# Optimization experiments

Measured on AMD Instinct MI355X. Metric: run time of the kernel, lower is better.

Reference implementation:

```python
import jax, jax.numpy as jnp
import numpy as np

EPS = 1e-6
NUM_HEADS = 16

def layernorm(x, alpha, bias):
    # Faithful to the torch module: torch.std uses ddof=1, and eps is added to std.
    mean = jnp.mean(x, axis=-1, keepdims=True)
    std = jnp.std(x, axis=-1, keepdims=True, ddof=1)
    return alpha * (x - mean) / (std + EPS) + bias

def setup_inputs() -> dict:
    key = jax.random.key(0)
    B, S, D, F = 4, 2048, 1024, 4096
    ks = jax.random.split(key, 8)
    s = 1.0 / np.sqrt(D)
    inp = {
        'x': jax.random.normal(ks[0], (B, S, D), jnp.float32),
        'src_mask': jnp.ones((B, 1, 1, S), jnp.int32),
        'wq': jax.random.normal(ks[1], (D, D), jnp.float32) * s,
        'bq': jnp.zeros((D,), jnp.float32),
        'wk': jax.random.normal(ks[2], (D, D), jnp.float32) * s,
        'bk': jnp.zeros((D,), jnp.float32),
        'wv': jax.random.normal(ks[3], (D, D), jnp.float32) * s,
        'bv': jnp.zeros((D,), jnp.float32),
        'wo': jax.random.normal(ks[4], (D, D), jnp.float32) * s,
        'bo': jnp.zeros((D,), jnp.float32),
        'w1': jax.random.normal(ks[5], (D, F), jnp.float32) * s,
        'b1': jnp.zeros((F,), jnp.float32),
        'w2': jax.random.normal(ks[6], (F, D), jnp.float32) * (1.0 / np.sqrt(F)),
        'b2': jnp.zeros((D,), jnp.float32),
        'ln1_a': jnp.ones((D,), jnp.float32),
        'ln1_b': jnp.zeros((D,), jnp.float32),
        'ln2_a': jnp.ones((D,), jnp.float32),
        'ln2_b': jnp.zeros((D,), jnp.float32),
    }
    return inp

def mha(x, src_mask, wq, bq, wk, bk, wv, bv, wo, bo):
    B, S, D = x.shape
    H = NUM_HEADS
    dk = D // H
    q = (x @ wq + bq).reshape(B, S, H, dk).transpose(0, 2, 1, 3)  # [B,H,S,dk]
    k = (x @ wk + bk).reshape(B, S, H, dk).transpose(0, 2, 1, 3)
    v = (x @ wv + bv).reshape(B, S, H, dk).transpose(0, 2, 1, 3)
    scores = jnp.einsum('bhqd,bhkd->bhqk', q, k) / np.sqrt(dk)  # [B,H,S,S]
    scores = jnp.where(src_mask == 0, -1e9, scores)
    p = jax.nn.softmax(scores, axis=-1)
    ctx = jnp.einsum('bhqk,bhkd->bhqd', p, v)  # [B,H,S,dk]
    ctx = ctx.transpose(0, 2, 1, 3).reshape(B, S, D)
    return ctx @ wo + bo

def reference(x, src_mask, wq, bq, wk, bk, wv, bv, wo, bo,
              w1, b1, w2, b2, ln1_a, ln1_b, ln2_a, ln2_b):
    # residual 1: pre-norm self-attention (dropout is identity in eval)
    h = x + mha(layernorm(x, ln1_a, ln1_b), src_mask, wq, bq, wk, bk, wv, bv, wo, bo)
    # residual 2: pre-norm FFN
    hn = layernorm(h, ln2_a, ln2_b)
    ffn = jax.nn.relu(hn @ w1 + b1) @ w2 + b2
    return h + ffn
```

## Files before the change

kernel.cpp:

```cpp
#include <hip/hip_runtime.h>
#include <hip/hip_bf16.h>

typedef __attribute__((ext_vector_type(8))) short bf16x8;
typedef __attribute__((ext_vector_type(4))) short bf16x4;
typedef __attribute__((ext_vector_type(4))) float f32x4;
typedef __hip_bfloat16 bf16;
typedef unsigned short u16;

#define B_ 4
#define S_ 2048
#define D_ 1024
#define F_ 4096
#define H_ 16
#define MROWS 8192

__device__ __forceinline__ u16 f2bf_bits(float f){
  union{bf16 h; u16 u;} x; x.h = __float2bfloat16(f); return x.u;
}
__device__ __forceinline__ unsigned packbf(float a, float b){
  return (unsigned)f2bf_bits(a) | ((unsigned)f2bf_bits(b)<<16);
}
__device__ __forceinline__ void gll16(const bf16* gp, u16* lp){
  __builtin_amdgcn_global_load_lds(
      (const __attribute__((address_space(1))) void*)gp,
      (__attribute__((address_space(3))) void*)lp, 16, 0, 0);
}

struct Ptr4 { const float* p[4]; };
__global__ __launch_bounds__(256) void transpose4_to_bf16(
    Ptr4 ws_, bf16* __restrict__ WT)
{
  __shared__ float t[32][33];
  const float* W = ws_.p[blockIdx.z];
  bf16* dst = WT + (size_t)blockIdx.z*1024*1024;
  int n0 = blockIdx.x*32, k0 = blockIdx.y*32;
  int x = threadIdx.x, y = threadIdx.y;
  #pragma unroll
  for (int i=0;i<32;i+=8)
    t[y+i][x] = W[(size_t)(k0+y+i)*1024 + n0+x];
  __syncthreads();
  #pragma unroll
  for (int i=0;i<32;i+=8)
    dst[(size_t)(n0+y+i)*1024 + k0+x] = __float2bfloat16(t[x][y+i]);
}

__global__ __launch_bounds__(256) void transpose_to_bf16(
    const float* __restrict__ W, bf16* __restrict__ WT, int K, int N)
{
  __shared__ float t[32][33];
  int n0 = blockIdx.x*32, k0 = blockIdx.y*32;
  int x = threadIdx.x, y = threadIdx.y;
  #pragma unroll
  for (int i=0;i<32;i+=8)
    t[y+i][x] = W[(size_t)(k0+y+i)*N + n0+x];
  __syncthreads();
  #pragma unroll
  for (int i=0;i<32;i+=8)
    WT[(size_t)(n0+y+i)*K + k0+x] = __float2bfloat16(t[x][y+i]);
}

__global__ __launch_bounds__(256) void concat_bias(
    const float* __restrict__ bq, const float* __restrict__ bk,
    const float* __restrict__ bv, float* __restrict__ out)
{
  int i = blockIdx.x*256 + threadIdx.x;
  float v = (i < 1024) ? bq[i] : (i < 2048) ? bk[i-1024] : bv[i-2048];
  out[i] = v;
}

__global__ __launch_bounds__(256) void v_transpose(
    const bf16* __restrict__ qkv, bf16* __restrict__ vT)
{
  __shared__ u16 tile[64*65];
  const int bh = blockIdx.y, b = bh>>4, h = bh&15;
  const int s0 = blockIdx.x*64;
  const int tid = threadIdx.x;
  const bf16* src = qkv + (size_t)(b*S_ + s0)*3072 + 2048 + h*64;
  #pragma unroll
  for (int i=0;i<2;i++){
    int idx = i*256 + tid;
    int r = idx>>3, sg = idx&7;
    uint4 v = *reinterpret_cast<const uint4*>(src + (size_t)r*3072 + sg*8);
    const u16* e = (const u16*)&v;
    #pragma unroll
    for (int j=0;j<8;j++) tile[r*65 + sg*8 + j] = e[j];
  }
  __syncthreads();
  bf16* dst = vT + (size_t)bh*64*S_ + s0;
  #pragma unroll
  for (int i=0;i<2;i++){
    int idx = i*256 + tid;
    int d = idx>>3, sg = idx&7;
    u16 tmp[8];
    #pragma unroll
    for (int j=0;j<8;j++) tmp[j] = tile[(sg*8+j)*65 + d];
    *reinterpret_cast<uint4*>(dst + (size_t)d*S_ + sg*8) = *reinterpret_cast<uint4*>(tmp);
  }
}

__device__ __forceinline__ float block_reduce_256(float v, float* sbuf){
  #pragma unroll
  for (int o=32;o>0;o>>=1) v += __shfl_down(v, o);
  int wave = threadIdx.x>>6;
  if ((threadIdx.x&63)==0) sbuf[wave] = v;
  __syncthreads();
  float r = sbuf[0]+sbuf[1]+sbuf[2]+sbuf[3];
  __syncthreads();
  return r;
}

__global__ __launch_bounds__(256) void ln_fwd(
    const float* __restrict__ x, const float* __restrict__ alpha,
    const float* __restrict__ beta, bf16* __restrict__ out)
{
  __shared__ float sbuf[4];
  int row = blockIdx.x, tid = threadIdx.x;
  const float4* xr = reinterpret_cast<const float4*>(x + (size_t)row*D_);
  float4 v = xr[tid];
  float sum = block_reduce_256(v.x+v.y+v.z+v.w, sbuf);
  float mean = sum * (1.0f/1024.0f);
  float dx0=v.x-mean, dx1=v.y-mean, dx2=v.z-mean, dx3=v.w-mean;
  float ssq = block_reduce_256(dx0*dx0+dx1*dx1+dx2*dx2+dx3*dx3, sbuf);
  float std_ = sqrtf(ssq * (1.0f/1023.0f));
  float inv = 1.0f/(std_ + 1e-6f);
  const float4* ar = reinterpret_cast<const float4*>(alpha);
  const float4* br = reinterpret_cast<const float4*>(beta);
  float4 a = ar[tid], bb = br[tid];
  unsigned* o = reinterpret_cast<unsigned*>(out + (size_t)row*D_);
  o[tid*2+0] = packbf(a.x*dx0*inv + bb.x, a.y*dx1*inv + bb.y);
  o[tid*2+1] = packbf(a.z*dx2*inv + bb.z, a.w*dx3*inv + bb.w);
}

template<int EPI, int TN>
__global__ __launch_bounds__(256) void gemm_bt(
    const bf16* __restrict__ A, const bf16* __restrict__ BT,
    const float* __restrict__ bias, const float* __restrict__ res,
    void* __restrict__ out, int M, int N, int K)
{
  constexpr int NWAVE = (TN == 128) ? 2 : 1;
  constexpr int NT = TN/64 + 1;
  __shared__ __align__(16) u16 As[128*32];
  __shared__ __align__(16) u16 Bs[TN*32];
  const int tid = threadIdx.x;
  const int m0 = blockIdx.x*128, n0 = blockIdx.y*TN;
  const int wave = tid>>6, lane = tid&63;
  const int wm = (wave>>1)*64, wn = (wave&1)*(TN/2);
  const int lrow = lane&15, quad = lane>>4;
  constexpr int BNT = TN/32;
  const int srow = wave*32 + (lane>>2);
  const int sseg = lane&3;
  const bf16* apg = A + (size_t)(m0+srow)*K + sseg*8;
  u16* asd = &As[wave*1024];
  const int brow = wave*(TN/4) + (lane>>2);
  const bf16* bpg = BT + (size_t)(n0+brow)*K + sseg*8;
  u16* bsd = &Bs[wave*(TN*8)];

  f32x4 acc[4][BNT];
  #pragma unroll
  for (int i=0;i<4;i++)
    #pragma unroll
    for (int j=0;j<BNT;j++) acc[i][j] = (f32x4){0.f,0.f,0.f,0.f};

  for (int k0=0; k0<K; k0+=32) {
    gll16(apg + k0,                 asd);
    gll16(apg + k0 + (size_t)16*K,  asd + 512);
    gll16(bpg + k0,                 bsd);
    if (TN == 128) gll16(bpg + k0 + (size_t)16*K, bsd + 512);
    __syncthreads();
    bf16x8 a[4], b[BNT];
    #pragma unroll
    for (int t=0;t<4;t++)
      a[t] = *reinterpret_cast<const bf16x8*>(&As[(wm + t*16 + lrow)*32 + quad*8]);
    #pragma unroll
    for (int t=0;t<BNT;t++)
      b[t] = *reinterpret_cast<const bf16x8*>(&Bs[(wn + t*16 + lrow)*32 + quad*8]);
    #pragma unroll
    for (int mt=0;mt<4;mt++)
      #pragma unroll
      for (int nt=0;nt<BNT;nt++)
        acc[mt][nt] = __builtin_amdgcn_mfma_f32_16x16x32_bf16(a[mt], b[nt], acc[mt][nt], 0,0,0);
    __syncthreads();
  }

  #pragma unroll
  for (int mt=0;mt<4;mt++){
    #pragma unroll
    for (int nt=0;nt<BNT;nt++){
      int col = n0 + wn + nt*16 + lrow;
      float bv = bias[col];
      #pragma unroll
      for (int r=0;r<4;r++){
        int row = m0 + wm + mt*16 + quad*4 + r;
        size_t idx = (size_t)row*N + col;
        float val = acc[mt][nt][r] + bv;
        if (EPI == 1) val = fmaxf(val, 0.0f);
        if (EPI == 2) {
          ((float*)out)[idx] = val + res[idx];
        } else {
          ((bf16*)out)[idx] = __float2bfloat16(val);
        }
      }
    }
  }
}

#define KP 72

__global__ __launch_bounds__(512) void flash_attn_mfma(
    const bf16* __restrict__ qkv, const bf16* __restrict__ vT,
    const int* __restrict__ mask, bf16* __restrict__ ctx)
{
  __shared__ __align__(16) u16 Ks[64*KP];
  __shared__ __align__(16) u16 Vt[64*KP];
  __shared__ __align__(16) float Mb[64];

  const int b = blockIdx.z, h = blockIdx.y, qt = blockIdx.x;
  const int tid = threadIdx.x, wave = tid>>6, lane = tid&63;
  const int lr = lane&15, quad = lane>>4;
  const int qbase = qt*256 + wave*32;

  const bf16* base = qkv + (size_t)b*S_*3072 + h*64;
  const bf16* vtb  = vT + (size_t)(b*H_+h)*64*S_;
  const int*  mrow = mask + b*S_;

  bf16x8 qf[2][2];
  #pragma unroll
  for (int c=0;c<2;c++){
    const bf16* qp = base + (size_t)(qbase + c*16 + lr)*3072 + quad*8;
    qf[c][0] = *reinterpret_cast<const bf16x8*>(qp);
    qf[c][1] = *reinterpret_cast<const bf16x8*>(qp + 32);
  }

  f32x4 actx[2][4];
  #pragma unroll
  for (int c=0;c<2;c++)
    #pragma unroll
    for (int dt=0;dt<4;dt++) actx[c][dt] = (f32x4){0.f,0.f,0.f,0.f};
  float lsum[2] = {0.f,0.f};

  const int sr = tid>>3, sg = tid&7;

  for (int kt=0; kt<S_; kt+=64){
    *reinterpret_cast<uint4*>(&Ks[sr*KP + sg*8]) =
      *reinterpret_cast<const uint4*>(base + 1024 + (size_t)(kt+sr)*3072 + sg*8);
    *reinterpret_cast<uint4*>(&Vt[sr*KP + sg*8]) =
      *reinterpret_cast<const uint4*>(vtb + (size_t)sr*S_ + kt + sg*8);
    if (tid < 64) Mb[tid] = (mrow[kt+tid]==0) ? -2e9f : 0.0f;
    __syncthreads();

    bf16x4 pk[2][4];
    #pragma unroll
    for (int nt=0;nt<4;nt++){
      bf16x8 kf0 = *reinterpret_cast<const bf16x8*>(&Ks[(nt*16+lr)*KP + quad*8]);
      bf16x8 kf1 = *reinterpret_cast<const bf16x8*>(&Ks[(nt*16+lr)*KP + 32 + quad*8]);
      float4 mb = *reinterpret_cast<const float4*>(&Mb[nt*16 + quad*4]);
      float mbv[4] = {mb.x, mb.y, mb.z, mb.w};
      #pragma unroll
      for (int c=0;c<2;c++){
        f32x4 a = (f32x4){0.f,0.f,0.f,0.f};
        a = __builtin_amdgcn_mfma_f32_16x16x32_bf16(kf0, qf[c][0], a, 0,0,0);
        a = __builtin_amdgcn_mfma_f32_16x16x32_bf16(kf1, qf[c][1], a, 0,0,0);
        u16 eb[4];
        #pragma unroll
        for (int r=0;r<4;r++){
          float e = exp2f(fmaf(a[r], 0.18033688011116012f, mbv[r]));
          lsum[c] += e;
          eb[r] = f2bf_bits(e);
        }
        bf16x4 t; t[0]=(short)eb[0]; t[1]=(short)eb[1]; t[2]=(short)eb[2]; t[3]=(short)eb[3];
        pk[c][nt] = t;
      }
    }

    #pragma unroll
    for (int dt=0;dt<4;dt++){
      #pragma unroll
      for (int kc=0;kc<4;kc++){
        bf16x4 vf = *reinterpret_cast<const bf16x4*>(&Vt[(dt*16+lr)*KP + kc*16 + quad*4]);
        #pragma unroll
        for (int c=0;c<2;c++)
          actx[c][dt] = __builtin_amdgcn_mfma_f32_16x16x16bf16_1k(vf, pk[c][kc], actx[c][dt], 0,0,0);
      }
    }
    __syncthreads();
  }

  #pragma unroll
  for (int c=0;c<2;c++){
    float l = lsum[c];
    l += __shfl_xor(l, 16);
    l += __shfl_xor(l, 32);
    float inv = 1.0f/l;
    int q = qbase + c*16 + lr;
    bf16* op = ctx + (size_t)(b*S_+q)*D_ + h*64 + quad*4;
    #pragma unroll
    for (int dt=0;dt<4;dt++){
      uint2 o;
      o.x = packbf(actx[c][dt][0]*inv, actx[c][dt][1]*inv);
      o.y = packbf(actx[c][dt][2]*inv, actx[c][dt][3]*inv);
      *reinterpret_cast<uint2*>(op + dt*16) = o;
    }
  }
}

extern "C" void kernel_launch(void* const* d_in, const int* in_sizes, int n_in,
                              void* d_out, int out_size, void* d_ws, size_t ws_size,
                              hipStream_t stream) {
  const float* x    = (const float*)d_in[0];
  const int*   mask = (const int*)  d_in[1];
  const float* wq   = (const float*)d_in[2];
  const float* bq   = (const float*)d_in[3];
  const float* wk   = (const float*)d_in[4];
  const float* bk   = (const float*)d_in[5];
  const float* wv   = (const float*)d_in[6];
  const float* bv   = (const float*)d_in[7];
  const float* wo   = (const float*)d_in[8];
  const float* bo   = (const float*)d_in[9];
  const float* w1   = (const float*)d_in[10];
  const float* b1   = (const float*)d_in[11];
  const float* w2   = (const float*)d_in[12];
  const float* b2   = (const float*)d_in[13];
  const float* ln1a = (const float*)d_in[14];
  const float* ln1b = (const float*)d_in[15];
  const float* ln2a = (const float*)d_in[16];
  const float* ln2b = (const float*)d_in[17];

  char* ws = (char*)d_ws;
  bf16*  wqkvT = (bf16*) (ws + 0);
  bf16*  woT   = (bf16*) (ws + 6291456);
  bf16*  w1T   = (bf16*) (ws + 8388608);
  bf16*  w2T   = (bf16*) (ws + 16777216);
  float* bqkv  = (float*)(ws + 25165824);
  bf16*  xn    = (bf16*) (ws + 25178112);
  bf16*  vT    = (bf16*) (ws + 25178112);
  bf16*  qkv   = (bf16*) (ws + 41955328);
  bf16*  ctx   = (bf16*) (ws + 92286976);
  bf16*  hn    = (bf16*) (ws + 109064192);
  bf16*  act   = (bf16*) (ws + 25178112);

  dim3 tb(32,8);
  Ptr4 wp; wp.p[0]=wq; wp.p[1]=wk; wp.p[2]=wv; wp.p[3]=wo;
  transpose4_to_bf16<<<dim3(32,32,4),tb,0,stream>>>(wp, wqkvT);
  transpose_to_bf16<<<dim3(128,32),tb,0,stream>>>(w1, w1T, 1024,4096);
  transpose_to_bf16<<<dim3(32,128),tb,0,stream>>>(w2, w2T, 4096,1024);
  concat_bias<<<12,256,0,stream>>>(bq,bk,bv,bqkv);

  ln_fwd<<<8192,256,0,stream>>>(x, ln1a, ln1b, xn);
  gemm_bt<0,128><<<dim3(64,24),256,0,stream>>>(xn, wqkvT, bqkv, nullptr, qkv, MROWS,3072,1024);
  v_transpose<<<dim3(32,64),256,0,stream>>>(qkv, vT);
  flash_attn_mfma<<<dim3(S_/256,H_,B_),512,0,stream>>>(qkv, vT, mask, ctx);
  gemm_bt<2,64><<<dim3(64,16),256,0,stream>>>(ctx, woT, bo, x, d_out, MROWS,1024,1024);
  ln_fwd<<<8192,256,0,stream>>>((const float*)d_out, ln2a, ln2b, hn);
  gemm_bt<1,128><<<dim3(64,32),256,0,stream>>>(hn, w1T, b1, nullptr, act, MROWS,F_,1024);
  gemm_bt<2,64><<<dim3(64,16),256,0,stream>>>(act, w2T, b2, (const float*)d_out, d_out, MROWS,1024,F_);
}
```

Before: 600.4 us.

## Fold softmax scale into QKV GEMM, skip mask when unmasked, MFMA row sums

Folds the softmax scale into the QKV projection epilogue for the Q columns, so attention scores go straight into a raw exp2 without an fma. Adds a wave ballot that takes a mask-free path when no key in the tile is masked. Computes the softmax denominator with an extra MFMA against a vector of ones instead of scalar adds and shuffles. Replaces the library bf16 conversion with a bit-trick pack; this rounds half-up rather than to nearest-even and adds extra MFMA work per tile.

```diff
diff --git a/kernel.cpp b/kernel.cpp
--- a/kernel.cpp
+++ b/kernel.cpp
@@ -13,12 +13,14 @@
 #define F_ 4096
 #define H_ 16
 #define MROWS 8192
-
+#define QSCALE 0.18033688011116012f
+
+__device__ __forceinline__ unsigned pkbf(float lo, float hi){
+  union{float f; unsigned u;} a, b; a.f = lo; b.f = hi;
+  return __builtin_amdgcn_perm(b.u + 0x8000u, a.u + 0x8000u, 0x07060302);
+}
 __device__ __forceinline__ u16 f2bf_bits(float f){
   union{bf16 h; u16 u;} x; x.h = __float2bfloat16(f); return x.u;
-}
-__device__ __forceinline__ unsigned packbf(float a, float b){
-  return (unsigned)f2bf_bits(a) | ((unsigned)f2bf_bits(b)<<16);
 }
 __device__ __forceinline__ void gll16(const bf16* gp, u16* lp){
   __builtin_amdgcn_global_load_lds(
@@ -127,8 +129,8 @@
   const float4* br = reinterpret_cast<const float4*>(beta);
   float4 a = ar[tid], bb = br[tid];
   unsigned* o = reinterpret_cast<unsigned*>(out + (size_t)row*D_);
-  o[tid*2+0] = packbf(a.x*dx0*inv + bb.x, a.y*dx1*inv + bb.y);
-  o[tid*2+1] = packbf(a.z*dx2*inv + bb.z, a.w*dx3*inv + bb.w);
+  o[tid*2+0] = pkbf(a.x*dx0*inv + bb.x, a.y*dx1*inv + bb.y);
+  o[tid*2+1] = pkbf(a.z*dx2*inv + bb.z, a.w*dx3*inv + bb.w);
 }
 
 template<int EPI, int TN>
@@ -137,8 +139,6 @@
     const float* __restrict__ bias, const float* __restrict__ res,
     void* __restrict__ out, int M, int N, int K)
 {
-  constexpr int NWAVE = (TN == 128) ? 2 : 1;
-  constexpr int NT = TN/64 + 1;
   __shared__ __align__(16) u16 As[128*32];
   __shared__ __align__(16) u16 Bs[TN*32];
   const int tid = threadIdx.x;
@@ -188,12 +188,14 @@
     for (int nt=0;nt<BNT;nt++){
       int col = n0 + wn + nt*16 + lrow;
       float bv = bias[col];
+      float sc = (EPI == 3 && col < 1024) ? QSCALE : 1.0f;
       #pragma unroll
       for (int r=0;r<4;r++){
         int row = m0 + wm + mt*16 + quad*4 + r;
         size_t idx = (size_t)row*N + col;
         float val = acc[mt][nt][r] + bv;
         if (EPI == 1) val = fmaxf(val, 0.0f);
+        if (EPI == 3) val *= sc;
         if (EPI == 2) {
           ((float*)out)[idx] = val + res[idx];
         } else {
@@ -231,12 +233,16 @@
     qf[c][1] = *reinterpret_cast<const bf16x8*>(qp + 32);
   }
 
+  const bf16x4 ones4 = {(short)0x3F80,(short)0x3F80,(short)0x3F80,(short)0x3F80};
+
   f32x4 actx[2][4];
-  #pragma unroll
-  for (int c=0;c<2;c++)
+  f32x4 acc_l[2];
+  #pragma unroll
+  for (int c=0;c<2;c++){
     #pragma unroll
     for (int dt=0;dt<4;dt++) actx[c][dt] = (f32x4){0.f,0.f,0.f,0.f};
-  float lsum[2] = {0.f,0.f};
+    acc_l[c] = (f32x4){0.f,0.f,0.f,0.f};
+  }
 
   const int sr = tid>>3, sg = tid&7;
 
@@ -246,29 +252,44 @@
     *reinterpret_cast<uint4*>(&Vt[sr*KP + sg*8]) =
       *reinterpret_cast<const uint4*>(vtb + (size_t)sr*S_ + kt + sg*8);
     if (tid < 64) Mb[tid] = (mrow[kt+tid]==0) ? -2e9f : 0.0f;
+    unsigned long long bal = __ballot(mrow[kt + lane] == 0);
     __syncthreads();
 
     bf16x4 pk[2][4];
-    #pragma unroll
-    for (int nt=0;nt<4;nt++){
-      bf16x8 kf0 = *reinterpret_cast<const bf16x8*>(&Ks[(nt*16+lr)*KP + quad*8]);
-      bf16x8 kf1 = *reinterpret_cast<const bf16x8*>(&Ks[(nt*16+lr)*KP + 32 + quad*8]);
-      float4 mb = *reinterpret_cast<const float4*>(&Mb[nt*16 + quad*4]);
-      float mbv[4] = {mb.x, mb.y, mb.z, mb.w};
-      #pragma unroll
-      for (int c=0;c<2;c++){
-        f32x4 a = (f32x4){0.f,0.f,0.f,0.f};
-        a = __builtin_amdgcn_mfma_f32_16x16x32_bf16(kf0, qf[c][0], a, 0,0,0);
-        a = __builtin_amdgcn_mfma_f32_16x16x32_bf16(kf1, qf[c][1], a, 0,0,0);
-        u16 eb[4];
+    if (bal == 0ULL) {
+      #pragma unroll
+      for (int nt=0;nt<4;nt++){
+        bf16x8 kf0 = *reinterpret_cast<const bf16x8*>(&Ks[(nt*16+lr)*KP + quad*8]);
+        bf16x8 kf1 = *reinterpret_cast<const bf16x8*>(&Ks[(nt*16+lr)*KP + 32 + quad*8]);
         #pragma unroll
-        for (int r=0;r<4;r++){
-          float e = exp2f(fmaf(a[r], 0.18033688011116012f, mbv[r]));
-          lsum[c] += e;
-          eb[r] = f2bf_bits(e);
+        for (int c=0;c<2;c++){
+          f32x4 a = (f32x4){0.f,0.f,0.f,0.f};
+          a = __builtin_amdgcn_mfma_f32_16x16x32_bf16(kf0, qf[c][0], a, 0,0,0);
+          a = __builtin_amdgcn_mfma_f32_16x16x32_bf16(kf1, qf[c][1], a, 0,0,0);
+          uint2 w;
+          w.x = pkbf(__builtin_amdgcn_exp2f(a[0]), __builtin_amdgcn_exp2f(a[1]));
+          w.y = pkbf(__builtin_amdgcn_exp2f(a[2]), __builtin_amdgcn_exp2f(a[3]));
+          union{uint2 u; bf16x4 v;} cvt; cvt.u = w;
+          pk[c][nt] = cvt.v;
         }
-        bf16x4 t; t[0]=(short)eb[0]; t[1]=(short)eb[1]; t[2]=(short)eb[2]; t[3]=(short)eb[3];
-        pk[c][nt] = t;
+      }
+    } else {
+      #pragma unroll
+      for (int nt=0;nt<4;nt++){
+        bf16x8 kf0 = *reinterpret_cast<const bf16x8*>(&Ks[(nt*16+lr)*KP + quad*8]);
+        bf16x8 kf1 = *reinterpret_cast<const bf16x8*>(&Ks[(nt*16+lr)*KP + 32 + quad*8]);
+        float4 mb = *reinterpret_cast<const float4*>(&Mb[nt*16 + quad*4]);
+        #pragma unroll
+        for (int c=0;c<2;c++){
+          f32x4 a = (f32x4){0.f,0.f,0.f,0.f};
+          a = __builtin_amdgcn_mfma_f32_16x16x32_bf16(kf0, qf[c][0], a, 0,0,0);
+          a = __builtin_amdgcn_mfma_f32_16x16x32_bf16(kf1, qf[c][1], a, 0,0,0);
+          uint2 w;
+          w.x = pkbf(__builtin_amdgcn_exp2f(a[0]+mb.x), __builtin_amdgcn_exp2f(a[1]+mb.y));
+          w.y = pkbf(__builtin_amdgcn_exp2f(a[2]+mb.z), __builtin_amdgcn_exp2f(a[3]+mb.w));
+          union{uint2 u; bf16x4 v;} cvt; cvt.u = w;
+          pk[c][nt] = cvt.v;
+        }
       }
     }
 
@@ -282,22 +303,24 @@
           actx[c][dt] = __builtin_amdgcn_mfma_f32_16x16x16bf16_1k(vf, pk[c][kc], actx[c][dt], 0,0,0);
       }
     }
+    #pragma unroll
+    for (int kc=0;kc<4;kc++)
+      #pragma unroll
+      for (int c=0;c<2;c++)
+        acc_l[c] = __builtin_amdgcn_mfma_f32_16x16x16bf16_1k(ones4, pk[c][kc], acc_l[c], 0,0,0);
     __syncthreads();
   }
 
   #pragma unroll
   for (int c=0;c<2;c++){
-    float l = lsum[c];
-    l += __shfl_xor(l, 16);
-    l += __shfl_xor(l, 32);
-    float inv = 1.0f/l;
+    float inv = 1.0f/acc_l[c][0];
     int q = qbase + c*16 + lr;
     bf16* op = ctx + (size_t)(b*S_+q)*D_ + h*64 + quad*4;
     #pragma unroll
     for (int dt=0;dt<4;dt++){
       uint2 o;
-      o.x = packbf(actx[c][dt][0]*inv, actx[c][dt][1]*inv);
-      o.y = packbf(actx[c][dt][2]*inv, actx[c][dt][3]*inv);
+      o.x = pkbf(actx[c][dt][0]*inv, actx[c][dt][1]*inv);
+      o.y = pkbf(actx[c][dt][2]*inv, actx[c][dt][3]*inv);
       *reinterpret_cast<uint2*>(op + dt*16) = o;
     }
   }
@@ -346,7 +369,7 @@
   concat_bias<<<12,256,0,stream>>>(bq,bk,bv,bqkv);
 
   ln_fwd<<<8192,256,0,stream>>>(x, ln1a, ln1b, xn);
-  gemm_bt<0,128><<<dim3(64,24),256,0,stream>>>(xn, wqkvT, bqkv, nullptr, qkv, MROWS,3072,1024);
+  gemm_bt<3,128><<<dim3(64,24),256,0,stream>>>(xn, wqkvT, bqkv, nullptr, qkv, MROWS,3072,1024);
   v_transpose<<<dim3(32,64),256,0,stream>>>(qkv, vT);
   flash_attn_mfma<<<dim3(S_/256,H_,B_),512,0,stream>>>(qkv, vT, mask, ctx);
   gemm_bt<2,64><<<dim3(64,16),256,0,stream>>>(ctx, woT, bo, x, d_out, MROWS,1024,1024);
```

New measurement: 563.8 us. 1.06x faster.
